# Kernel tuning notes

Measured on AMD Instinct MI355X. Metric: run time of the kernel, lower is better.

## Reference

```python
import jax, jax.numpy as jnp
import numpy as np

N_SRC = 32768   # source-type nodes
N_DST = 32768   # predict-type nodes
N = N_SRC + N_DST
E = 524288      # pos-graph edges (src-type -> predict-type)
E_NEG = 419430
D_IN = 256
D_H = 256
EPS = 1e-8      # torch cosine_similarity eps


def setup_inputs() -> dict:
    key = jax.random.key(0)
    ks = jax.random.split(key, 6)
    feat = jax.random.normal(ks[0], (N, D_IN), jnp.float32)
    src = jax.random.randint(ks[1], (E,), 0, N_SRC, jnp.int32)
    dst = jax.random.randint(ks[2], (E,), 0, N_DST, jnp.int32) + N_SRC  # edges into predict partition
    perm = jax.random.permutation(ks[3], E)[:E_NEG]  # drop-edge fuse
    neg_src = src[perm]
    neg_dst = dst[perm]
    W = jax.random.normal(ks[4], (D_IN, D_H), jnp.float32) / np.float32(np.sqrt(D_IN))
    b = jnp.zeros((D_H,), jnp.float32)
    prelu_a = jnp.full((1,), 0.25, jnp.float32)  # PReLU default init
    return {"feat": feat, "src": src, "dst": dst, "neg_src": neg_src,
            "neg_dst": neg_dst, "W": W, "b": b, "prelu_a": prelu_a}


def _graph_conv(feat, src, dst, W, b, a):
    # DGL GraphConv(norm='right') on homogeneous graph with self-loops added:
    # h_v = PReLU( (sum_{u->v} x_u W) / in_deg(v) + b )
    loop = jnp.arange(N, dtype=src.dtype)
    s = jnp.concatenate([src, loop])
    d = jnp.concatenate([dst, loop])
    m = feat @ W                                   # [N, D_H]
    agg = jax.ops.segment_sum(m[s], d, num_segments=N)
    deg = jax.ops.segment_sum(jnp.ones_like(d, m.dtype), d, num_segments=N)
    h = agg / jnp.maximum(deg, 1.0)[:, None] + b
    return jnp.where(h >= 0, h, a * h)             # PReLU (single shared slope)


def _normalize(x):
    n = jnp.maximum(jnp.linalg.norm(x, axis=-1, keepdims=True), EPS)
    return x / n


def _seg_cos(anchor_n, nei_n, s, d):
    # per-edge cosine(anchor[dst], nei[src]) summed over in-edges of each predict node
    c = jnp.sum(anchor_n[d] * nei_n[s], axis=-1)
    mask = d >= N_SRC
    idx = jnp.where(mask, d - N_SRC, 0)
    return jax.ops.segment_sum(jnp.where(mask, c, jnp.zeros_like(c)), idx, num_segments=N_DST)


def reference(feat, src, dst, neg_src, neg_dst, W, b, prelu_a):
    h_pos = _graph_conv(feat, src, dst, W, b, prelu_a)
    h_neg = _graph_conv(feat, neg_src, neg_dst, W, b, prelu_a)
    hp = _normalize(h_pos)
    hn = _normalize(h_neg)
    # positive pairs: same predict node across the two views
    pos_loss = jnp.sum(hp[N_SRC:] * hn[N_SRC:], axis=-1)  # [N_DST]
    # neighbor sets include the self-loop (dgl.add_self_loop before the loss)
    loop = jnp.arange(N, dtype=src.dtype)
    ps, pd = jnp.concatenate([src, loop]), jnp.concatenate([dst, loop])
    ns, nd = jnp.concatenate([neg_src, loop]), jnp.concatenate([neg_dst, loop])
    neg_loss = jnp.concatenate([
        _seg_cos(hp, hn, ns, nd),   # pos anchors vs neg-graph in-neighbors
        _seg_cos(hn, hp, ps, pd),   # neg anchors vs pos-graph in-neighbors
    ])
    all_sim = jnp.concatenate([pos_loss, neg_loss])
    loss = jnp.log(jnp.sum(jnp.exp(all_sim))) - jnp.sum(pos_loss)
    return loss, h_pos[N_SRC:]
```

## Files before the change

kernel.cpp:

```cpp
#include <hip/hip_runtime.h>
#include <math.h>

#define NSRC 32768
#define NTOT 65536
#define NDST 32768
#define DH   256
#define SLOTS 64
#define CLBIT 0x80000000u

typedef __attribute__((ext_vector_type(8))) short bf16x8;
typedef __attribute__((ext_vector_type(4))) float f32x4;
typedef __attribute__((ext_vector_type(2))) float f32x2;

__device__ __forceinline__ float wave_reduce(float v) {
#pragma unroll
  for (int off = 32; off > 0; off >>= 1) v += __shfl_xor(v, off, 64);
  return v;
}
__device__ __forceinline__ unsigned short f2bf(float f) {
  union { float f; unsigned u; } v; v.f = f;
  unsigned r = v.u + 0x7FFFu + ((v.u >> 16) & 1u);
  return (unsigned short)(r >> 16);
}
__device__ __forceinline__ unsigned pk_fp8(float x, float y, float z, float w) {
  int v = __builtin_amdgcn_cvt_pk_fp8_f32(x, y, 0, false);
  v = __builtin_amdgcn_cvt_pk_fp8_f32(z, w, v, true);
  return (unsigned)v;
}
__device__ __forceinline__ float4 unpk_fp8(unsigned u) {
  f32x2 lo = __builtin_amdgcn_cvt_pk_f32_fp8((int)u, false);
  f32x2 hi = __builtin_amdgcn_cvt_pk_f32_fp8((int)u, true);
  return make_float4(lo[0], lo[1], hi[0], hi[1]);
}
__device__ __forceinline__ void add4(float4& a, const float4 v) {
  a.x += v.x; a.y += v.y; a.z += v.z; a.w += v.w;
}
__device__ __forceinline__ float4 sub4(const float4 a, const float4 v) {
  return make_float4(a.x - v.x, a.y - v.y, a.z - v.z, a.w - v.w);
}
__device__ __forceinline__ float dot4(const float4 a, const float4 b) {
  return a.x * b.x + a.y * b.y + a.z * b.z + a.w * b.w;
}
__device__ __forceinline__ float prelu1(float x, float a) {
  return fmaxf(x, 0.f) + a * fminf(x, 0.f);
}
__device__ __forceinline__ float4 hsrc4(const float4 v, const float4 bv,
                                        float alpha, float isc) {
  float4 h;
  h.x = prelu1(v.x + bv.x, alpha) * isc;
  h.y = prelu1(v.y + bv.y, alpha) * isc;
  h.z = prelu1(v.z + bv.z, alpha) * isc;
  h.w = prelu1(v.w + bv.w, alpha) * isc;
  return h;
}

__global__ __launch_bounds__(256) void k_prep(const float* __restrict__ W,
                                              unsigned short* __restrict__ Wt,
                                              const int* __restrict__ src,
                                              const int* __restrict__ dst,
                                              const int* __restrict__ ndst,
                                              int* __restrict__ cur,
                                              int* __restrict__ eSrc,
                                              int* __restrict__ degN,
                                              int nE, int nEn) {
  int bid = blockIdx.x;
  const int t = threadIdx.x;
  if (bid < 256) {
    Wt[bid * 256 + t] = f2bf(W[(size_t)t * 256 + bid]);
    return;
  }
  bid -= 256;
  const int nbP = (nE + 255) / 256;
  if (bid < nbP) {
    const int e = bid * 256 + t;
    if (e < nE) {
      const int d = dst[e] - NSRC;
      const int p = atomicAdd(&cur[d], 1);
      if (p < SLOTS) eSrc[d * SLOTS + p] = src[e];
    }
    return;
  }
  bid -= nbP;
  const int e = bid * 256 + t;
  if (e < nEn) atomicAdd(&degN[ndst[e] - NSRC], 1);
}

__global__ __launch_bounds__(512) void k_gemm(
    const float* __restrict__ A, const unsigned short* __restrict__ Wt,
    const float* __restrict__ b, const float* __restrict__ pa,
    unsigned* __restrict__ mb8, float* __restrict__ inn) {
  __shared__ unsigned short wl[16384];
  const int bid = blockIdx.x;
  const int t = threadIdx.x;
  const int lane = t & 63;
  const int wv = t >> 6;
  const int ln = lane & 15;
  const int kq = lane >> 4;
  const int row = bid * 128 + wv * 16 + ln;
  const bool is_src = (bid < 256);
  const float alpha = pa[0];

  bf16x8 bs[8];
  const float* ap = A + (size_t)row * 256 + kq * 8;
#pragma unroll
  for (int ks = 0; ks < 8; ++ks) {
    float4 a0 = *(const float4*)(ap + ks * 32);
    float4 a1 = *(const float4*)(ap + ks * 32 + 4);
    bf16x8 v;
    v[0] = (short)f2bf(a0.x); v[1] = (short)f2bf(a0.y);
    v[2] = (short)f2bf(a0.z); v[3] = (short)f2bf(a0.w);
    v[4] = (short)f2bf(a1.x); v[5] = (short)f2bf(a1.y);
    v[6] = (short)f2bf(a1.z); v[7] = (short)f2bf(a1.w);
    bs[ks] = v;
  }

  float ss = 0.f;
  for (int q = 0; q < 4; ++q) {
    __syncthreads();
#pragma unroll
    for (int r = 0; r < 4; ++r) {
      const int flat = r * 512 + t;
      const int f = flat >> 6;
      const int ls = flat & 63;
      const int n = q * 64 + (f >> 3) * 16 + (ls & 15);
      const int k = ((ls >> 4) << 3) + (f & 7) * 32;
      *(bf16x8*)(wl + flat * 8) = *(const bf16x8*)(Wt + (size_t)n * 256 + k);
    }
    __syncthreads();

    f32x4 acc[4];
#pragma unroll
    for (int i = 0; i < 4; ++i) acc[i] = (f32x4){0.f, 0.f, 0.f, 0.f};
#pragma unroll
    for (int nt = 0; nt < 4; ++nt) {
#pragma unroll
      for (int ks = 0; ks < 8; ++ks) {
        bf16x8 af = *(const bf16x8*)(wl + ((nt * 8 + ks) * 64 + lane) * 8);
        acc[nt] = __builtin_amdgcn_mfma_f32_16x16x32_bf16(af, bs[ks], acc[nt], 0, 0, 0);
      }
    }
#pragma unroll
    for (int nt = 0; nt < 4; ++nt) {
      mb8[(size_t)row * 64 + q * 16 + nt * 4 + kq] =
          pk_fp8(acc[nt][0], acc[nt][1], acc[nt][2], acc[nt][3]);
      if (is_src) {
        const int n0 = q * 64 + nt * 16 + kq * 4;
        float4 bv = *(const float4*)(b + n0);
        float hx = prelu1(acc[nt][0] + bv.x, alpha);
        float hy = prelu1(acc[nt][1] + bv.y, alpha);
        float hz = prelu1(acc[nt][2] + bv.z, alpha);
        float hw = prelu1(acc[nt][3] + bv.w, alpha);
        ss += hx * hx + hy * hy + hz * hz + hw * hw;
      }
    }
  }
  if (is_src) {
    ss += __shfl_xor(ss, 16, 64);
    ss += __shfl_xor(ss, 32, 64);
    if (kq == 0) inn[row] = 1.0f / fmaxf(sqrtf(ss), 1e-8f);
  }
}

__global__ __launch_bounds__(256) void k_claim(const int* __restrict__ nsrc,
                                               const int* __restrict__ ndst,
                                               const int* __restrict__ cur,
                                               int* __restrict__ eSrc, int nEn) {
  const int i = blockIdx.x * 256 + threadIdx.x;
  if (i >= nEn) return;
  const int d = ndst[i] - NSRC;
  const int s = nsrc[i];
  const int cnt = cur[d];
  const int base = d * SLOTS;
  int j = 0;
  for (; j + 3 < cnt; j += 4) {
    const int4 q = *(const int4*)(eSrc + base + j);
    if (q.x == s && atomicCAS((unsigned*)&eSrc[base + j],     (unsigned)s, s | CLBIT) == (unsigned)s) return;
    if (q.y == s && atomicCAS((unsigned*)&eSrc[base + j + 1], (unsigned)s, s | CLBIT) == (unsigned)s) return;
    if (q.z == s && atomicCAS((unsigned*)&eSrc[base + j + 2], (unsigned)s, s | CLBIT) == (unsigned)s) return;
    if (q.w == s && atomicCAS((unsigned*)&eSrc[base + j + 3], (unsigned)s, s | CLBIT) == (unsigned)s) return;
  }
  for (; j < cnt; ++j) {
    if (eSrc[base + j] == s &&
        atomicCAS((unsigned*)&eSrc[base + j], (unsigned)s, s | CLBIT) == (unsigned)s) return;
  }
}

__global__ __launch_bounds__(256) void k_fused(const unsigned* __restrict__ mb8,
                                               const float* __restrict__ inn,
                                               const int* __restrict__ cur,
                                               const int* __restrict__ eSrc,
                                               const int* __restrict__ degN,
                                               const float* __restrict__ b,
                                               const float* __restrict__ pa,
                                               float* __restrict__ hraw,
                                               float* __restrict__ sims) {
  const int row = blockIdx.x * 4 + (threadIdx.x >> 6);
  const int lane = threadIdx.x & 63;
  const int c = lane * 4;
  const int cnt = cur[row];
  const int base = row * SLOTS;
  const int cN = degN[row];
  const float4 bv = *(const float4*)(b + c);
  const float alpha = pa[0];
  const unsigned* mbl = mb8 + lane;

  float4 self = unpk_fp8(mbl[(size_t)(NSRC + row) * 64]);
  float4 aP0 = self, aP1 = {0.f, 0.f, 0.f, 0.f};
  float4 sP0 = {0.f, 0.f, 0.f, 0.f}, sP1 = {0.f, 0.f, 0.f, 0.f};
  float4 aU0 = {0.f, 0.f, 0.f, 0.f}, aU1 = {0.f, 0.f, 0.f, 0.f};
  float4 sU0 = {0.f, 0.f, 0.f, 0.f}, sU1 = {0.f, 0.f, 0.f, 0.f};

  int e = 0;
  for (; e + 3 < cnt; e += 4) {
    const int4 ev = *(const int4*)(eSrc + base + e);
    const int s0 = ev.x & 0x7fffffff, s1 = ev.y & 0x7fffffff;
    const int s2 = ev.z & 0x7fffffff, s3 = ev.w & 0x7fffffff;
    const unsigned r0 = mbl[(size_t)s0 * 64];
    const unsigned r1 = mbl[(size_t)s1 * 64];
    const unsigned r2 = mbl[(size_t)s2 * 64];
    const unsigned r3 = mbl[(size_t)s3 * 64];
    const float i0 = inn[s0], i1 = inn[s1], i2 = inn[s2], i3 = inn[s3];
    float4 v0 = unpk_fp8(r0), v1 = unpk_fp8(r1);
    float4 v2 = unpk_fp8(r2), v3 = unpk_fp8(r3);
    float4 h0 = hsrc4(v0, bv, alpha, i0);
    float4 h1 = hsrc4(v1, bv, alpha, i1);
    float4 h2 = hsrc4(v2, bv, alpha, i2);
    float4 h3 = hsrc4(v3, bv, alpha, i3);
    add4(aP0, v0); add4(aP1, v1); add4(aP0, v2); add4(aP1, v3);
    add4(sP0, h0); add4(sP1, h1); add4(sP0, h2); add4(sP1, h3);
    if (ev.x >= 0) { add4(aU0, v0); add4(sU0, h0); }
    if (ev.y >= 0) { add4(aU1, v1); add4(sU1, h1); }
    if (ev.z >= 0) { add4(aU0, v2); add4(sU0, h2); }
    if (ev.w >= 0) { add4(aU1, v3); add4(sU1, h3); }
  }
  for (; e < cnt; ++e) {
    const int ev = eSrc[base + e];
    const int s0 = ev & 0x7fffffff;
    const float i0 = inn[s0];
    float4 v0 = unpk_fp8(mbl[(size_t)s0 * 64]);
    float4 h0 = hsrc4(v0, bv, alpha, i0);
    add4(aP0, v0); add4(sP0, h0);
    if (ev >= 0) { add4(aU0, v0); add4(sU0, h0); }
  }
  add4(aP0, aP1); add4(sP0, sP1); add4(aU0, aU1); add4(sU0, sU1);
  float4 aN0 = sub4(aP0, aU0);
  float4 sN0 = sub4(sP0, sU0);

  const float invP = 1.0f / (float)(cnt + 1);
  const float invN = 1.0f / (float)(cN + 1);
  float4 hp, hn;
  hp.x = prelu1(aP0.x * invP + bv.x, alpha);
  hp.y = prelu1(aP0.y * invP + bv.y, alpha);
  hp.z = prelu1(aP0.z * invP + bv.z, alpha);
  hp.w = prelu1(aP0.w * invP + bv.w, alpha);
  hn.x = prelu1(aN0.x * invN + bv.x, alpha);
  hn.y = prelu1(aN0.y * invN + bv.y, alpha);
  hn.z = prelu1(aN0.z * invN + bv.z, alpha);
  hn.w = prelu1(aN0.w * invN + bv.w, alpha);

  *(float4*)(hraw + (size_t)row * 256 + c) = hp;

  float ssP = wave_reduce(dot4(hp, hp));
  float ssN = wave_reduce(dot4(hn, hn));
  const float iP = 1.0f / fmaxf(sqrtf(ssP), 1e-8f);
  const float iN = 1.0f / fmaxf(sqrtf(ssN), 1e-8f);
  float4 xp = hp, xn = hn;
  xp.x *= iP; xp.y *= iP; xp.z *= iP; xp.w *= iP;
  xn.x *= iN; xn.y *= iN; xn.z *= iN; xn.w *= iN;

  float pos = wave_reduce(dot4(xp, xn));
  float n1 = wave_reduce(dot4(xp, sN0));
  float n2 = wave_reduce(dot4(xn, sP0));
  if (lane == 0) {
    sims[row] = pos;
    sims[NDST + row] = pos + n1;
    sims[2 * NDST + row] = pos + n2;
  }
}

__global__ __launch_bounds__(256) void k_reduce(const float* __restrict__ sims,
                                                float* __restrict__ red,
                                                int* __restrict__ ticket,
                                                float* __restrict__ out,
                                                int nblocks) {
  const int i = blockIdx.x * 256 + threadIdx.x;
  const float v = sims[i];
  float e = expf(v);
  float p = (i < NDST) ? v : 0.f;
  e = wave_reduce(e);
  p = wave_reduce(p);
  __shared__ float se[4], sp[4];
  const int lane = threadIdx.x & 63, w = threadIdx.x >> 6;
  if (lane == 0) { se[w] = e; sp[w] = p; }
  __syncthreads();
  if (threadIdx.x == 0) {
    atomicAdd(red + 0, se[0] + se[1] + se[2] + se[3]);
    atomicAdd(red + 1, sp[0] + sp[1] + sp[2] + sp[3]);
    __threadfence();
    const int old = atomicAdd(ticket, 1);
    if (old == nblocks - 1) {
      const float s = atomicAdd(red + 0, 0.0f);
      const float q = atomicAdd(red + 1, 0.0f);
      out[0] = logf(s) - q;
    }
  }
}

extern "C" void kernel_launch(void* const* d_in, const int* in_sizes, int n_in,
                              void* d_out, int out_size, void* d_ws, size_t ws_size,
                              hipStream_t stream) {
  const float* feat = (const float*)d_in[0];
  const int*   src  = (const int*)d_in[1];
  const int*   dst  = (const int*)d_in[2];
  const int*   nsrc = (const int*)d_in[3];
  const int*   ndst = (const int*)d_in[4];
  const float* W    = (const float*)d_in[5];
  const float* b    = (const float*)d_in[6];
  const float* pa   = (const float*)d_in[7];
  const int nE  = in_sizes[1];
  const int nEn = in_sizes[3];
  float* out = (float*)d_out;

  unsigned* mb8 = (unsigned*)d_ws;
  unsigned short* Wt = (unsigned short*)(mb8 + (size_t)NTOT * 64);
  float* inn  = (float*)(Wt + 256 * 256);
  float* sims = inn + NSRC;
  int* eSrc = (int*)(sims + 3 * (size_t)NDST);
  int* cur  = eSrc + (size_t)NDST * SLOTS;
  int* degN = cur + NDST;
  float* red = (float*)(degN + NDST);
  int* ticket = (int*)(red + 4);
  const size_t zero_bytes = (2 * (size_t)NDST + 8) * 4;

  hipMemsetAsync(cur, 0, zero_bytes, stream);

  const int nbP = (nE + 255) / 256, nbN = (nEn + 255) / 256;
  k_prep<<<256 + nbP + nbN, 256, 0, stream>>>(W, Wt, src, dst, ndst, cur, eSrc,
                                              degN, nE, nEn);
  k_gemm<<<512, 512, 0, stream>>>(feat, Wt, b, pa, mb8, inn);
  k_claim<<<nbN, 256, 0, stream>>>(nsrc, ndst, cur, eSrc, nEn);
  k_fused<<<NDST / 4, 256, 0, stream>>>(mb8, inn, cur, eSrc, degN, b, pa,
                                        out + 1, sims);
  const int nbR = (3 * NDST) / 256;
  k_reduce<<<nbR, 256, 0, stream>>>(sims, red, ticket, out, nbR);
}
```

Before: 186.4 us.

## Replace atomic claim kernel with wave-ballot matching of negative edges in fused kernel

The separate k_claim pass, which used atomicCAS to mark pos-graph slots that also appear in the negative graph, is removed. The prep kernel now buckets negative-graph sources per destination into a second slot array. The fused kernel matches them against the lane-held pos slots with wave ballots to build a claim mask. This saves a kernel launch and the scattered atomic traffic, at the cost of a serial ballot loop per row and extra workspace. The bf16 conversion also switches to the library intrinsic.

```diff
diff --git a/kernel.cpp b/kernel.cpp
--- a/kernel.cpp
+++ b/kernel.cpp
@@ -1,4 +1,5 @@
 #include <hip/hip_runtime.h>
+#include <hip/hip_bf16.h>
 #include <math.h>
 
 #define NSRC 32768
@@ -6,7 +7,6 @@
 #define NDST 32768
 #define DH   256
 #define SLOTS 64
-#define CLBIT 0x80000000u
 
 typedef __attribute__((ext_vector_type(8))) short bf16x8;
 typedef __attribute__((ext_vector_type(4))) float f32x4;
@@ -18,9 +18,8 @@
   return v;
 }
 __device__ __forceinline__ unsigned short f2bf(float f) {
-  union { float f; unsigned u; } v; v.f = f;
-  unsigned r = v.u + 0x7FFFu + ((v.u >> 16) & 1u);
-  return (unsigned short)(r >> 16);
+  __hip_bfloat16 h = __float2bfloat16(f);
+  return __builtin_bit_cast(unsigned short, h);
 }
 __device__ __forceinline__ unsigned pk_fp8(float x, float y, float z, float w) {
   int v = __builtin_amdgcn_cvt_pk_fp8_f32(x, y, 0, false);
@@ -58,10 +57,12 @@
                                               unsigned short* __restrict__ Wt,
                                               const int* __restrict__ src,
                                               const int* __restrict__ dst,
+                                              const int* __restrict__ nsrc,
                                               const int* __restrict__ ndst,
                                               int* __restrict__ cur,
                                               int* __restrict__ eSrc,
                                               int* __restrict__ degN,
+                                              int* __restrict__ eSrcN,
                                               int nE, int nEn) {
   int bid = blockIdx.x;
   const int t = threadIdx.x;
@@ -82,7 +83,11 @@
   }
   bid -= nbP;
   const int e = bid * 256 + t;
-  if (e < nEn) atomicAdd(&degN[ndst[e] - NSRC], 1);
+  if (e < nEn) {
+    const int d = ndst[e] - NSRC;
+    const int p = atomicAdd(&degN[d], 1);
+    if (p < SLOTS) eSrcN[d * SLOTS + p] = nsrc[e];
+  }
 }
 
 __global__ __launch_bounds__(512) void k_gemm(
@@ -161,35 +166,12 @@
   }
 }
 
-__global__ __launch_bounds__(256) void k_claim(const int* __restrict__ nsrc,
-                                               const int* __restrict__ ndst,
-                                               const int* __restrict__ cur,
-                                               int* __restrict__ eSrc, int nEn) {
-  const int i = blockIdx.x * 256 + threadIdx.x;
-  if (i >= nEn) return;
-  const int d = ndst[i] - NSRC;
-  const int s = nsrc[i];
-  const int cnt = cur[d];
-  const int base = d * SLOTS;
-  int j = 0;
-  for (; j + 3 < cnt; j += 4) {
-    const int4 q = *(const int4*)(eSrc + base + j);
-    if (q.x == s && atomicCAS((unsigned*)&eSrc[base + j],     (unsigned)s, s | CLBIT) == (unsigned)s) return;
-    if (q.y == s && atomicCAS((unsigned*)&eSrc[base + j + 1], (unsigned)s, s | CLBIT) == (unsigned)s) return;
-    if (q.z == s && atomicCAS((unsigned*)&eSrc[base + j + 2], (unsigned)s, s | CLBIT) == (unsigned)s) return;
-    if (q.w == s && atomicCAS((unsigned*)&eSrc[base + j + 3], (unsigned)s, s | CLBIT) == (unsigned)s) return;
-  }
-  for (; j < cnt; ++j) {
-    if (eSrc[base + j] == s &&
-        atomicCAS((unsigned*)&eSrc[base + j], (unsigned)s, s | CLBIT) == (unsigned)s) return;
-  }
-}
-
 __global__ __launch_bounds__(256) void k_fused(const unsigned* __restrict__ mb8,
                                                const float* __restrict__ inn,
                                                const int* __restrict__ cur,
                                                const int* __restrict__ eSrc,
                                                const int* __restrict__ degN,
+                                               const int* __restrict__ eSrcN,
                                                const float* __restrict__ b,
                                                const float* __restrict__ pa,
                                                float* __restrict__ hraw,
@@ -204,6 +186,23 @@
   const float alpha = pa[0];
   const unsigned* mbl = mb8 + lane;
 
+  const int myslot = (lane < cnt) ? eSrc[base + lane] : -1;
+  bool claimed = false;
+  for (int i = 0; i < cN; i += 4) {
+    const int4 sv = *(const int4*)(eSrcN + base + i);
+#pragma unroll
+    for (int u = 0; u < 4; ++u) {
+      if (i + u >= cN) break;
+      const int s = (u == 0) ? sv.x : (u == 1) ? sv.y : (u == 2) ? sv.z : sv.w;
+      const unsigned long long cand = __ballot(!claimed && myslot == s);
+      if (cand) {
+        const int first = __ffsll(cand) - 1;
+        claimed = claimed || (lane == first);
+      }
+    }
+  }
+  const unsigned long long claimmask = __ballot(claimed);
+
   float4 self = unpk_fp8(mbl[(size_t)(NSRC + row) * 64]);
   float4 aP0 = self, aP1 = {0.f, 0.f, 0.f, 0.f};
   float4 sP0 = {0.f, 0.f, 0.f, 0.f}, sP1 = {0.f, 0.f, 0.f, 0.f};
@@ -213,13 +212,12 @@
   int e = 0;
   for (; e + 3 < cnt; e += 4) {
     const int4 ev = *(const int4*)(eSrc + base + e);
-    const int s0 = ev.x & 0x7fffffff, s1 = ev.y & 0x7fffffff;
-    const int s2 = ev.z & 0x7fffffff, s3 = ev.w & 0x7fffffff;
-    const unsigned r0 = mbl[(size_t)s0 * 64];
-    const unsigned r1 = mbl[(size_t)s1 * 64];
-    const unsigned r2 = mbl[(size_t)s2 * 64];
-    const unsigned r3 = mbl[(size_t)s3 * 64];
-    const float i0 = inn[s0], i1 = inn[s1], i2 = inn[s2], i3 = inn[s3];
+    const unsigned r0 = mbl[(size_t)ev.x * 64];
+    const unsigned r1 = mbl[(size_t)ev.y * 64];
+    const unsigned r2 = mbl[(size_t)ev.z * 64];
+    const unsigned r3 = mbl[(size_t)ev.w * 64];
+    const float i0 = inn[ev.x], i1 = inn[ev.y];
+    const float i2 = inn[ev.z], i3 = inn[ev.w];
     float4 v0 = unpk_fp8(r0), v1 = unpk_fp8(r1);
     float4 v2 = unpk_fp8(r2), v3 = unpk_fp8(r3);
     float4 h0 = hsrc4(v0, bv, alpha, i0);
@@ -228,19 +226,18 @@
     float4 h3 = hsrc4(v3, bv, alpha, i3);
     add4(aP0, v0); add4(aP1, v1); add4(aP0, v2); add4(aP1, v3);
     add4(sP0, h0); add4(sP1, h1); add4(sP0, h2); add4(sP1, h3);
-    if (ev.x >= 0) { add4(aU0, v0); add4(sU0, h0); }
-    if (ev.y >= 0) { add4(aU1, v1); add4(sU1, h1); }
-    if (ev.z >= 0) { add4(aU0, v2); add4(sU0, h2); }
-    if (ev.w >= 0) { add4(aU1, v3); add4(sU1, h3); }
+    if (!((claimmask >> e) & 1))       { add4(aU0, v0); add4(sU0, h0); }
+    if (!((claimmask >> (e + 1)) & 1)) { add4(aU1, v1); add4(sU1, h1); }
+    if (!((claimmask >> (e + 2)) & 1)) { add4(aU0, v2); add4(sU0, h2); }
+    if (!((claimmask >> (e + 3)) & 1)) { add4(aU1, v3); add4(sU1, h3); }
   }
   for (; e < cnt; ++e) {
-    const int ev = eSrc[base + e];
-    const int s0 = ev & 0x7fffffff;
+    const int s0 = eSrc[base + e];
     const float i0 = inn[s0];
     float4 v0 = unpk_fp8(mbl[(size_t)s0 * 64]);
     float4 h0 = hsrc4(v0, bv, alpha, i0);
     add4(aP0, v0); add4(sP0, h0);
-    if (ev >= 0) { add4(aU0, v0); add4(sU0, h0); }
+    if (!((claimmask >> e) & 1)) { add4(aU0, v0); add4(sU0, h0); }
   }
   add4(aP0, aP1); add4(sP0, sP1); add4(aU0, aU1); add4(sU0, sU1);
   float4 aN0 = sub4(aP0, aU0);
@@ -325,8 +322,9 @@
   unsigned short* Wt = (unsigned short*)(mb8 + (size_t)NTOT * 64);
   float* inn  = (float*)(Wt + 256 * 256);
   float* sims = inn + NSRC;
-  int* eSrc = (int*)(sims + 3 * (size_t)NDST);
-  int* cur  = eSrc + (size_t)NDST * SLOTS;
+  int* eSrc  = (int*)(sims + 3 * (size_t)NDST);
+  int* eSrcN = eSrc + (size_t)NDST * SLOTS;
+  int* cur  = eSrcN + (size_t)NDST * SLOTS;
   int* degN = cur + NDST;
   float* red = (float*)(degN + NDST);
   int* ticket = (int*)(red + 4);
@@ -335,11 +333,10 @@
   hipMemsetAsync(cur, 0, zero_bytes, stream);
 
   const int nbP = (nE + 255) / 256, nbN = (nEn + 255) / 256;
-  k_prep<<<256 + nbP + nbN, 256, 0, stream>>>(W, Wt, src, dst, ndst, cur, eSrc,
-                                              degN, nE, nEn);
+  k_prep<<<256 + nbP + nbN, 256, 0, stream>>>(W, Wt, src, dst, nsrc, ndst, cur,
+                                              eSrc, degN, eSrcN, nE, nEn);
   k_gemm<<<512, 512, 0, stream>>>(feat, Wt, b, pa, mb8, inn);
-  k_claim<<<nbN, 256, 0, stream>>>(nsrc, ndst, cur, eSrc, nEn);
-  k_fused<<<NDST / 4, 256, 0, stream>>>(mb8, inn, cur, eSrc, degN, b, pa,
+  k_fused<<<NDST / 4, 256, 0, stream>>>(mb8, inn, cur, eSrc, degN, eSrcN, b, pa,
                                         out + 1, sims);
   const int nbR = (3 * NDST) / 256;
   k_reduce<<<nbR, 256, 0, stream>>>(sims, red, ticket, out, nbR);
```

After: 198.9 us. 6.7% more time.

## Split GEMM by output quarter with 256-row tiles and atomic norm accumulation

Applied to the files above, without the earlier changes.

The GEMM kernel now launches 1024 blocks. Each block computes one 64-column quarter of the output for 256 rows, two 16-row subtiles per wave, and loads its W slice into shared memory only once instead of looping over four quarters with two barriers each. The per-row squared-norm partials for source nodes are combined with float atomics into a zeroed buffer, and the inverse norm is computed in extra blocks appended to the claim kernel. It also switches to the library bf16 conversion. In exchange, each block re-reads its A rows, so A is read four times overall, and it adds atomics and a larger memset.

```diff
diff --git a/kernel.cpp b/kernel.cpp
--- a/kernel.cpp
+++ b/kernel.cpp
@@ -1,4 +1,5 @@
 #include <hip/hip_runtime.h>
+#include <hip/hip_bf16.h>
 #include <math.h>
 
 #define NSRC 32768
@@ -18,9 +19,8 @@
   return v;
 }
 __device__ __forceinline__ unsigned short f2bf(float f) {
-  union { float f; unsigned u; } v; v.f = f;
-  unsigned r = v.u + 0x7FFFu + ((v.u >> 16) & 1u);
-  return (unsigned short)(r >> 16);
+  __hip_bfloat16 h = __float2bfloat16(f);
+  return __builtin_bit_cast(unsigned short, h);
 }
 __device__ __forceinline__ unsigned pk_fp8(float x, float y, float z, float w) {
   int v = __builtin_amdgcn_cvt_pk_fp8_f32(x, y, 0, false);
@@ -88,84 +88,109 @@
 __global__ __launch_bounds__(512) void k_gemm(
     const float* __restrict__ A, const unsigned short* __restrict__ Wt,
     const float* __restrict__ b, const float* __restrict__ pa,
-    unsigned* __restrict__ mb8, float* __restrict__ inn) {
+    unsigned* __restrict__ mb8, float* __restrict__ ssacc) {
   __shared__ unsigned short wl[16384];
   const int bid = blockIdx.x;
+  const int rowgrp = (bid & 7) | ((bid >> 5) << 3);
+  const int quarter = (bid >> 3) & 3;
   const int t = threadIdx.x;
   const int lane = t & 63;
   const int wv = t >> 6;
   const int ln = lane & 15;
   const int kq = lane >> 4;
-  const int row = bid * 128 + wv * 16 + ln;
-  const bool is_src = (bid < 256);
+  const int row0 = rowgrp * 256 + wv * 32 + ln;
+  const bool is_src = (rowgrp < 128);
   const float alpha = pa[0];
 
-  bf16x8 bs[8];
-  const float* ap = A + (size_t)row * 256 + kq * 8;
-#pragma unroll
-  for (int ks = 0; ks < 8; ++ks) {
-    float4 a0 = *(const float4*)(ap + ks * 32);
-    float4 a1 = *(const float4*)(ap + ks * 32 + 4);
-    bf16x8 v;
-    v[0] = (short)f2bf(a0.x); v[1] = (short)f2bf(a0.y);
-    v[2] = (short)f2bf(a0.z); v[3] = (short)f2bf(a0.w);
-    v[4] = (short)f2bf(a1.x); v[5] = (short)f2bf(a1.y);
-    v[6] = (short)f2bf(a1.z); v[7] = (short)f2bf(a1.w);
-    bs[ks] = v;
-  }
-
-  float ss = 0.f;
-  for (int q = 0; q < 4; ++q) {
-    __syncthreads();
-#pragma unroll
-    for (int r = 0; r < 4; ++r) {
-      const int flat = r * 512 + t;
-      const int f = flat >> 6;
-      const int ls = flat & 63;
-      const int n = q * 64 + (f >> 3) * 16 + (ls & 15);
-      const int k = ((ls >> 4) << 3) + (f & 7) * 32;
-      *(bf16x8*)(wl + flat * 8) = *(const bf16x8*)(Wt + (size_t)n * 256 + k);
-    }
-    __syncthreads();
-
-    f32x4 acc[4];
-#pragma unroll
-    for (int i = 0; i < 4; ++i) acc[i] = (f32x4){0.f, 0.f, 0.f, 0.f};
+  bf16x8 bs[2][8];
+#pragma unroll
+  for (int s = 0; s < 2; ++s) {
+    const float* ap = A + (size_t)(row0 + s * 16) * 256 + kq * 8;
+#pragma unroll
+    for (int ks = 0; ks < 8; ++ks) {
+      float4 a0 = *(const float4*)(ap + ks * 32);
+      float4 a1 = *(const float4*)(ap + ks * 32 + 4);
+      bf16x8 v;
+      v[0] = (short)f2bf(a0.x); v[1] = (short)f2bf(a0.y);
+      v[2] = (short)f2bf(a0.z); v[3] = (short)f2bf(a0.w);
+      v[4] = (short)f2bf(a1.x); v[5] = (short)f2bf(a1.y);
+      v[6] = (short)f2bf(a1.z); v[7] = (short)f2bf(a1.w);
+      bs[s][ks] = v;
+    }
+  }
+
+#pragma unroll
+  for (int r = 0; r < 4; ++r) {
+    const int flat = r * 512 + t;
+    const int f = flat >> 6;
+    const int ls = flat & 63;
+    const int n = quarter * 64 + (f >> 3) * 16 + (ls & 15);
+    const int k = ((ls >> 4) << 3) + (f & 7) * 32;
+    *(bf16x8*)(wl + flat * 8) = *(const bf16x8*)(Wt + (size_t)n * 256 + k);
+  }
+  __syncthreads();
+
+  f32x4 acc[2][4];
+#pragma unroll
+  for (int s = 0; s < 2; ++s)
+#pragma unroll
+    for (int i = 0; i < 4; ++i) acc[s][i] = (f32x4){0.f, 0.f, 0.f, 0.f};
+
+#pragma unroll
+  for (int nt = 0; nt < 4; ++nt) {
+#pragma unroll
+    for (int ks = 0; ks < 8; ++ks) {
+      bf16x8 af = *(const bf16x8*)(wl + ((nt * 8 + ks) * 64 + lane) * 8);
+      acc[0][nt] = __builtin_amdgcn_mfma_f32_16x16x32_bf16(af, bs[0][ks], acc[0][nt], 0, 0, 0);
+      acc[1][nt] = __builtin_amdgcn_mfma_f32_16x16x32_bf16(af, bs[1][ks], acc[1][nt], 0, 0, 0);
+    }
+  }
+
+  float ss[2] = {0.f, 0.f};
+#pragma unroll
+  for (int s = 0; s < 2; ++s)
 #pragma unroll
     for (int nt = 0; nt < 4; ++nt) {
-#pragma unroll
-      for (int ks = 0; ks < 8; ++ks) {
-        bf16x8 af = *(const bf16x8*)(wl + ((nt * 8 + ks) * 64 + lane) * 8);
-        acc[nt] = __builtin_amdgcn_mfma_f32_16x16x32_bf16(af, bs[ks], acc[nt], 0, 0, 0);
+      const int row = row0 + s * 16;
+      mb8[(size_t)row * 64 + quarter * 16 + nt * 4 + kq] =
+          pk_fp8(acc[s][nt][0], acc[s][nt][1], acc[s][nt][2], acc[s][nt][3]);
+      if (is_src) {
+        const int n0 = quarter * 64 + nt * 16 + kq * 4;
+        float4 bv = *(const float4*)(b + n0);
+        float hx = prelu1(acc[s][nt][0] + bv.x, alpha);
+        float hy = prelu1(acc[s][nt][1] + bv.y, alpha);
+        float hz = prelu1(acc[s][nt][2] + bv.z, alpha);
+        float hw = prelu1(acc[s][nt][3] + bv.w, alpha);
+        ss[s] += hx * hx + hy * hy + hz * hz + hw * hw;
       }
     }
-#pragma unroll
-    for (int nt = 0; nt < 4; ++nt) {
-      mb8[(size_t)row * 64 + q * 16 + nt * 4 + kq] =
-          pk_fp8(acc[nt][0], acc[nt][1], acc[nt][2], acc[nt][3]);
-      if (is_src) {
-        const int n0 = q * 64 + nt * 16 + kq * 4;
-        float4 bv = *(const float4*)(b + n0);
-        float hx = prelu1(acc[nt][0] + bv.x, alpha);
-        float hy = prelu1(acc[nt][1] + bv.y, alpha);
-        float hz = prelu1(acc[nt][2] + bv.z, alpha);
-        float hw = prelu1(acc[nt][3] + bv.w, alpha);
-        ss += hx * hx + hy * hy + hz * hz + hw * hw;
-      }
-    }
-  }
   if (is_src) {
-    ss += __shfl_xor(ss, 16, 64);
-    ss += __shfl_xor(ss, 32, 64);
-    if (kq == 0) inn[row] = 1.0f / fmaxf(sqrtf(ss), 1e-8f);
+#pragma unroll
+    for (int s = 0; s < 2; ++s) {
+      ss[s] += __shfl_xor(ss[s], 16, 64);
+      ss[s] += __shfl_xor(ss[s], 32, 64);
+    }
+    if (kq == 0) {
+      atomicAdd(&ssacc[row0], ss[0]);
+      atomicAdd(&ssacc[row0 + 16], ss[1]);
+    }
   }
 }
 
 __global__ __launch_bounds__(256) void k_claim(const int* __restrict__ nsrc,
                                                const int* __restrict__ ndst,
                                                const int* __restrict__ cur,
-                                               int* __restrict__ eSrc, int nEn) {
-  const int i = blockIdx.x * 256 + threadIdx.x;
+                                               int* __restrict__ eSrc, int nEn,
+                                               const float* __restrict__ ssacc,
+                                               float* __restrict__ inn) {
+  int bid = blockIdx.x;
+  const int nbC = (nEn + 255) / 256;
+  if (bid >= nbC) {
+    const int row = (bid - nbC) * 256 + threadIdx.x;
+    inn[row] = 1.0f / fmaxf(sqrtf(ssacc[row]), 1e-8f);
+    return;
+  }
+  const int i = bid * 256 + threadIdx.x;
   if (i >= nEn) return;
   const int d = ndst[i] - NSRC;
   const int s = nsrc[i];
@@ -330,15 +355,17 @@
   int* degN = cur + NDST;
   float* red = (float*)(degN + NDST);
   int* ticket = (int*)(red + 4);
-  const size_t zero_bytes = (2 * (size_t)NDST + 8) * 4;
+  float* ssacc = (float*)(ticket + 4);
+  const size_t zero_bytes = (2 * (size_t)NDST + 8 + NSRC) * 4;
 
   hipMemsetAsync(cur, 0, zero_bytes, stream);
 
   const int nbP = (nE + 255) / 256, nbN = (nEn + 255) / 256;
   k_prep<<<256 + nbP + nbN, 256, 0, stream>>>(W, Wt, src, dst, ndst, cur, eSrc,
                                               degN, nE, nEn);
-  k_gemm<<<512, 512, 0, stream>>>(feat, Wt, b, pa, mb8, inn);
-  k_claim<<<nbN, 256, 0, stream>>>(nsrc, ndst, cur, eSrc, nEn);
+  k_gemm<<<1024, 512, 0, stream>>>(feat, Wt, b, pa, mb8, ssacc);
+  k_claim<<<nbN + NSRC / 256, 256, 0, stream>>>(nsrc, ndst, cur, eSrc, nEn,
+                                                ssacc, inn);
   k_fused<<<NDST / 4, 256, 0, stream>>>(mb8, inn, cur, eSrc, degN, b, pa,
                                         out + 1, sims);
   const int nbR = (3 * NDST) / 256;
```

Result: slower. 201.4 us (+8.0%).
